# Kernel optimization log

Measured on AMD Instinct MI355X. Metric: run time of the kernel, lower is better.

## Reference

```python
import jax, jax.numpy as jnp
import numpy as np

N_NODES = 100000
IN_CH, HID_CH, OUT_CH = 128, 128, 64
N_EDGES = 1600000


def _gcn_conv(x, W, b, src, dst, num_nodes):
    """PyG GCNConv with gcn_norm(add_self_loops=True): adds one self-loop per
    node to the given edge set, symmetric deg^-1/2 normalization, then
    gather-scale-scatter of the linearly transformed features."""
    loop = jnp.arange(num_nodes)
    s = jnp.concatenate([src, loop])
    d = jnp.concatenate([dst, loop])
    # degree over targets (flow source_to_target), edge weights = 1
    deg = jax.ops.segment_sum(jnp.ones_like(s, x.dtype), d, num_segments=num_nodes)
    dinv = jnp.where(deg > 0, deg ** -0.5, 0.0)
    norm = dinv[s] * dinv[d]                      # [E']
    h = x @ W                                     # [N, out]
    msg = h[s] * norm[:, None]                    # [E', out] gather + scale
    out = jax.ops.segment_sum(msg, d, num_segments=num_nodes)  # scatter-add
    return out + b


def setup_inputs() -> dict:
    key = jax.random.key(0)
    k = jax.random.split(key, 6)
    x = jax.random.normal(k[0], (N_NODES, IN_CH), dtype=jnp.float32)
    edge_index = jax.random.randint(k[1], (2, N_EDGES), 0, N_NODES, dtype=jnp.int64)
    # Glorot-scale params
    W1 = jax.random.normal(k[2], (IN_CH, HID_CH), dtype=jnp.float32) * (2.0 / (IN_CH + HID_CH)) ** 0.5
    b1 = jnp.zeros((HID_CH,), dtype=jnp.float32)
    W2 = jax.random.normal(k[3], (HID_CH, OUT_CH), dtype=jnp.float32) * (2.0 / (HID_CH + OUT_CH)) ** 0.5
    b2 = jnp.zeros((OUT_CH,), dtype=jnp.float32)
    return {"x": x, "edge_index": edge_index, "W1": W1, "b1": b1, "W2": W2, "b2": b2}


def reference(x, edge_index, W1, b1, W2, b2):
    num_nodes = x.shape[0]
    loop = jnp.arange(num_nodes, dtype=edge_index.dtype)
    # wrapper-level add_self_loops (GCNConv adds another internally)
    src = jnp.concatenate([edge_index[0], loop])
    dst = jnp.concatenate([edge_index[1], loop])
    h = _gcn_conv(x, W1, b1, src, dst, num_nodes)
    h = jax.nn.relu(h)
    h = _gcn_conv(h, W2, b2, src, dst, num_nodes)
    return jax.nn.log_softmax(h, axis=1)
```

## Files before the change

kernel.cpp:

```cpp
#include <hip/hip_runtime.h>
#include <cstdint>
#include <cstddef>

#define IN_CH 128
#define HID_CH 128
#define OUT_CH 64
#define BSH 8
#define PB 4096
#define CAP 6144

typedef unsigned int uint32;
typedef unsigned char uchar;
typedef short bf16x8 __attribute__((ext_vector_type(8)));
typedef float f32x4 __attribute__((ext_vector_type(4)));
typedef float f32x2 __attribute__((ext_vector_type(2)));

static __device__ __forceinline__ unsigned short f2bf(float f) {
    uint32 u = __float_as_uint(f);
    u += 0x7fffu + ((u >> 16) & 1u);
    return (unsigned short)(u >> 16);
}

typedef const __attribute__((address_space(1))) char gch;
typedef __attribute__((address_space(3))) char lch;
static __device__ __forceinline__ void gload16(const void* g, void* l) {
    __builtin_amdgcn_global_load_lds((gch*)g, (lch*)l, 16, 0, 0);
}


__global__ __launch_bounds__(256) void part1_wtrans(
    const int* __restrict__ src, const int* __restrict__ dst,
    int* __restrict__ bcur, int2* __restrict__ pairBuf, int E, int NB, int gP,
    const float* __restrict__ W1, const float* __restrict__ W2,
    unsigned short* __restrict__ W1t, unsigned short* __restrict__ W2t) {
    if (blockIdx.x >= (uint32)gP) {
        int t = (blockIdx.x - gP) * 256 + threadIdx.x;
        if (t < 128 * 128) {
            int nc = t >> 7, k = t & 127;
            W1t[t] = f2bf(W1[k * 128 + nc]);
        }
        int u = t - 128 * 128;
        if (u >= 0 && u < 64 * 128) {
            int nc = u >> 7, k = u & 127;
            W2t[u] = f2bf(W2[k * 64 + nc]);
        }
        return;
    }
    __shared__ int2 pairs[PB];
    __shared__ int hist[512];
    __shared__ int base[512];
    int t = threadIdx.x;
    int e0 = blockIdx.x * PB;
    int cnt = min(PB, E - e0);
    for (int b = t; b < NB; b += 256) hist[b] = 0;
    __syncthreads();
    for (int i = t; i < cnt; i += 256) {
        int s = src[e0 + i], d = dst[e0 + i];
        pairs[i] = make_int2(s, d);
        atomicAdd(&hist[d >> BSH], 1);
    }
    __syncthreads();
    for (int b = t; b < NB; b += 256) {
        int h = hist[b];
        int gb = (h > 0) ? atomicAdd(&bcur[b], h) : 0;
        base[b] = b * CAP + gb;
        hist[b] = 0;
    }
    __syncthreads();
    for (int i = t; i < cnt; i += 256) {
        int2 p = pairs[i];
        int b = p.y >> BSH;
        int q = base[b] + atomicAdd(&hist[b], 1);
        pairBuf[q] = p;
    }
}

__global__ __launch_bounds__(256) void bucket_build(
    const int2* __restrict__ pairBuf, const int* __restrict__ bcur,
    int* __restrict__ rowptr, int* __restrict__ deg, float* __restrict__ dinv,
    int* __restrict__ csr, int N) {
    __shared__ int cnt[256];
    __shared__ int loc[256];
    int b = blockIdx.x, t = threadIdx.x;
    int start = b * CAP, end = start + bcur[b];
    cnt[t] = 0;
    __syncthreads();
    for (int i = start + t; i < end; i += 256)
        atomicAdd(&cnt[pairBuf[i].y & 255], 1);
    __syncthreads();
    int v = cnt[t];
    loc[t] = v;
    __syncthreads();
    for (int o = 1; o < 256; o <<= 1) {
        int add = (t >= o) ? loc[t - o] : 0;
        __syncthreads();
        loc[t] += add;
        __syncthreads();
    }
    int excl = loc[t] - v;
    int node = (b << BSH) + t;
    if (node < N) {
        rowptr[node] = start + excl;
        deg[node] = v;
        dinv[node] = rsqrtf((float)(v + 2));
    }
    __syncthreads();
    cnt[t] = excl;
    __syncthreads();
    for (int i = start + t; i < end; i += 256) {
        int2 p = pairBuf[i];
        int q = start + atomicAdd(&cnt[p.y & 255], 1);
        csr[q] = p.x;
    }
}


__global__ __launch_bounds__(256) void gemm1_mfma(
    const float* __restrict__ A, const unsigned short* __restrict__ Wt,
    const float* __restrict__ dinv, uchar* __restrict__ C, int n, int nTiles) {
    constexpr int NT = 8;
    constexpr int RP = 528;
    __shared__ unsigned short Ws[128 * 136];
    __shared__ char As[4 * 9216];

    const int t = threadIdx.x;

    for (int i = t; i < 128 * 16; i += 256) {
        int rr = i >> 4, sq = i & 15;
        *(uint4*)&Ws[rr * 136 + sq * 8] = *(const uint4*)(Wt + rr * 128 + sq * 8);
    }
    __syncthreads();

    const int w = t >> 6, l = t & 63;
    const int q = l >> 4, r16 = l & 15;
    char* slice = As + w * 9216;
    const char* myrow = slice + r16 * RP;

    for (int tile = blockIdx.x; tile < nTiles; tile += gridDim.x) {
        const int row0 = tile * 64 + w * 16;

#pragma unroll
        for (int rnd = 0; rnd < 9; rnd++) {
            int p = rnd * 1024 + l * 16;
            int row = p / RP;
            int col = (p - row * RP) & 511;
            int rg = min(row0 + min(row, 15), n - 1);
            gload16((const char*)A + (size_t)rg * 512 + col, slice + p);
        }
        asm volatile("s_waitcnt vmcnt(0)" ::: "memory");
        __builtin_amdgcn_sched_barrier(0);

        f32x4 acc[NT];
#pragma unroll
        for (int i = 0; i < NT; i++) acc[i] = (f32x4){0.f, 0.f, 0.f, 0.f};

#pragma unroll
        for (int s = 0; s < 4; s++) {
            const int k0 = s * 32 + q * 8;
            float4 v0 = *(const float4*)(myrow + k0 * 4);
            float4 v1 = *(const float4*)(myrow + k0 * 4 + 16);
            bf16x8 xf;
            xf[0] = (short)f2bf(v0.x); xf[1] = (short)f2bf(v0.y);
            xf[2] = (short)f2bf(v0.z); xf[3] = (short)f2bf(v0.w);
            xf[4] = (short)f2bf(v1.x); xf[5] = (short)f2bf(v1.y);
            xf[6] = (short)f2bf(v1.z); xf[7] = (short)f2bf(v1.w);
#pragma unroll
            for (int nt = 0; nt < NT; nt++) {
                bf16x8 wf = *(const bf16x8*)&Ws[(nt * 16 + r16) * 136 + k0];
                acc[nt] = __builtin_amdgcn_mfma_f32_16x16x32_bf16(wf, xf, acc[nt], 0, 0, 0);
            }
        }

        const int node = row0 + r16;
        const bool nv = node < n;
        const float dv = dinv[min(node, n - 1)];
        uchar* Crow = C + (size_t)node * 128;
#pragma unroll
        for (int nt = 0; nt < NT; nt++) {
            int pk = 0;
            pk = __builtin_amdgcn_cvt_pk_fp8_f32(acc[nt][0] * dv, acc[nt][1] * dv, pk, false);
            pk = __builtin_amdgcn_cvt_pk_fp8_f32(acc[nt][2] * dv, acc[nt][3] * dv, pk, true);
            if (nv) *(uint32*)(Crow + nt * 16 + q * 4) = (uint32)pk;
        }
    }
}


__global__ __launch_bounds__(256) void agg1_fused(
    const uchar* __restrict__ H, const int* __restrict__ csr,
    const int* __restrict__ rowptr, const int* __restrict__ deg,
    const float* __restrict__ dinv, const float* __restrict__ bias,
    const unsigned short* __restrict__ W2t, uchar* __restrict__ H2, int n) {
    __shared__ char stage[4][8192];
    __shared__ unsigned short tile[16 * 136];
    int t = threadIdx.x;
    int slot = t >> 4;
    int v = blockIdx.x * 16 + slot;
    int hl = t & 15;
    int gsel = t & 48;
    int w = t >> 6;
    int gg = (t >> 4) & 3;
    bool valid = v < n;
    int vc = valid ? v : 0;
    int base = rowptr[vc];
    int cnt = valid ? deg[vc] : 0;

    f32x2 A0 = (f32x2){0.f, 0.f}, A1 = A0, A2 = A0, A3 = A0;
    f32x2 B0 = A0, B1 = A0, B2 = A0, B3 = A0;

#define ACC128(h, s0, s1, s2, s3)                                   \
    {                                                               \
        s0 += __builtin_amdgcn_cvt_pk_f32_fp8((h).x, false);        \
        s1 += __builtin_amdgcn_cvt_pk_f32_fp8((h).x, true);         \
        s2 += __builtin_amdgcn_cvt_pk_f32_fp8((h).y, false);        \
        s3 += __builtin_amdgcn_cvt_pk_f32_fp8((h).y, true);         \
    }

    char* sl = stage[w];
    const char* rg = sl + gg * 256 + hl * 8;

    int ul = 0;
    if (hl < min(16, cnt)) ul = csr[base + hl];

    for (int j0 = 0; j0 < cnt; j0 += 16) {
        int nj = min(16, cnt - j0);
#pragma unroll
        for (int i = 0; i < 8; i++) {
            int j = i * 2 + (hl >> 3);
            int u = __shfl(ul, j | gsel);
            gload16(H + (((uint32)u << 7) + ((uint32)(hl & 7) << 4)),
                    sl + i * 1024);
        }
        int ul2 = 0;
        int j0n = j0 + 16;
        if (j0n < cnt && hl < min(16, cnt - j0n)) ul2 = csr[base + j0n + hl];
        asm volatile("s_waitcnt vmcnt(4)" ::: "memory");
        __builtin_amdgcn_sched_barrier(0);
#pragma unroll
        for (int j = 0; j < 8; j++) {
            if (j < nj) {
                uint2 h = *(const uint2*)(rg + (j >> 1) * 1024 + (j & 1) * 128);
                if (j & 1) { ACC128(h, B0, B1, B2, B3); }
                else       { ACC128(h, A0, A1, A2, A3); }
            }
        }
        asm volatile("s_waitcnt vmcnt(0)" ::: "memory");
        __builtin_amdgcn_sched_barrier(0);
#pragma unroll
        for (int j = 8; j < 16; j++) {
            if (j < nj) {
                uint2 h = *(const uint2*)(rg + (j >> 1) * 1024 + (j & 1) * 128);
                if (j & 1) { ACC128(h, B0, B1, B2, B3); }
                else       { ACC128(h, A0, A1, A2, A3); }
            }
        }
        ul = ul2;
    }
#undef ACC128

    const uint32 co = (uint32)(hl * 8);
    uint4 pk = make_uint4(0, 0, 0, 0);
    if (valid) {
        float dv = dinv[vc];
        uint2 hv = *(const uint2*)(H + (((uint32)vc << 7) + co));
        f32x2 s0 = __builtin_amdgcn_cvt_pk_f32_fp8(hv.x, false);
        f32x2 s1 = __builtin_amdgcn_cvt_pk_f32_fp8(hv.x, true);
        f32x2 s2 = __builtin_amdgcn_cvt_pk_f32_fp8(hv.y, false);
        f32x2 s3 = __builtin_amdgcn_cvt_pk_f32_fp8(hv.y, true);
        const f32x2* bp = (const f32x2*)(bias + hl * 8);
        f32x2 e0 = dv * ((A0 + B0) + 2.f * s0) + bp[0];
        f32x2 e1 = dv * ((A1 + B1) + 2.f * s1) + bp[1];
        f32x2 e2 = dv * ((A2 + B2) + 2.f * s2) + bp[2];
        f32x2 e3 = dv * ((A3 + B3) + 2.f * s3) + bp[3];
        float o0 = fmaxf(e0[0], 0.f), o1 = fmaxf(e0[1], 0.f);
        float o2 = fmaxf(e1[0], 0.f), o3 = fmaxf(e1[1], 0.f);
        float o4 = fmaxf(e2[0], 0.f), o5 = fmaxf(e2[1], 0.f);
        float o6 = fmaxf(e3[0], 0.f), o7 = fmaxf(e3[1], 0.f);
        pk.x = (uint32)f2bf(o0) | ((uint32)f2bf(o1) << 16);
        pk.y = (uint32)f2bf(o2) | ((uint32)f2bf(o3) << 16);
        pk.z = (uint32)f2bf(o4) | ((uint32)f2bf(o5) << 16);
        pk.w = (uint32)f2bf(o6) | ((uint32)f2bf(o7) << 16);
    }
    *(uint4*)&tile[slot * 136 + hl * 8] = pk;
    __syncthreads();

    const int l = t & 63;
    const int q = l >> 4, r16 = l & 15;
    f32x4 acc2 = (f32x4){0.f, 0.f, 0.f, 0.f};
#pragma unroll
    for (int s = 0; s < 4; s++) {
        const int k0 = s * 32 + q * 8;
        bf16x8 hf = *(const bf16x8*)&tile[r16 * 136 + k0];
        bf16x8 wf = *(const bf16x8*)(W2t + (size_t)(w * 16 + r16) * 128 + k0);
        acc2 = __builtin_amdgcn_mfma_f32_16x16x32_bf16(wf, hf, acc2, 0, 0, 0);
    }
    const int node = blockIdx.x * 16 + r16;
    if (node < n) {
        const float dv2 = dinv[node];
        int pk2 = 0;
        pk2 = __builtin_amdgcn_cvt_pk_fp8_f32(acc2[0] * dv2, acc2[1] * dv2, pk2, false);
        pk2 = __builtin_amdgcn_cvt_pk_fp8_f32(acc2[2] * dv2, acc2[3] * dv2, pk2, true);
        *(uint32*)(H2 + (size_t)node * 64 + w * 16 + q * 4) = (uint32)pk2;
    }
}

__global__ __launch_bounds__(256) void agg_lsm_64(
    const uchar* __restrict__ H, const int* __restrict__ csr,
    const int* __restrict__ rowptr, const int* __restrict__ deg,
    const float* __restrict__ dinv, const float* __restrict__ bias,
    float* __restrict__ out, int n) {
    __shared__ char stage[4][4096];
    int t = threadIdx.x;
    int v = blockIdx.x * 16 + (t >> 4);
    int hl = t & 15;
    int gsel = t & 48;
    int w = t >> 6;
    int gg = (t >> 4) & 3;
    bool valid = v < n;
    int vc = valid ? v : 0;
    int base = rowptr[vc];
    int cnt = valid ? deg[vc] : 0;
    const uint32 co = (uint32)(hl * 4);

    f32x2 A0 = (f32x2){0.f, 0.f}, A1 = A0, B0 = A0, B1 = A0;

#define ACC64(h, s0, s1)                                            \
    {                                                               \
        s0 += __builtin_amdgcn_cvt_pk_f32_fp8((h), false);          \
        s1 += __builtin_amdgcn_cvt_pk_f32_fp8((h), true);           \
    }

    char* sl = stage[w];
    const char* rg = sl + gg * 256 + hl * 4;

    int ul = 0;
    if (hl < min(16, cnt)) ul = csr[base + hl];

    for (int j0 = 0; j0 < cnt; j0 += 16) {
        int nj = min(16, cnt - j0);
#pragma unroll
        for (int i = 0; i < 4; i++) {
            int j = i * 4 + (hl >> 2);
            int u = __shfl(ul, j | gsel);
            gload16(H + (((uint32)u << 6) + ((uint32)(hl & 3) << 4)),
                    sl + i * 1024);
        }
        int ul2 = 0;
        int j0n = j0 + 16;
        if (j0n < cnt && hl < min(16, cnt - j0n)) ul2 = csr[base + j0n + hl];
        asm volatile("s_waitcnt vmcnt(2)" ::: "memory");
        __builtin_amdgcn_sched_barrier(0);
#pragma unroll
        for (int j = 0; j < 8; j++) {
            if (j < nj) {
                uint32 h = *(const uint32*)(rg + (j >> 2) * 1024 + (j & 3) * 64);
                if (j & 1) { ACC64(h, B0, B1); }
                else       { ACC64(h, A0, A1); }
            }
        }
        asm volatile("s_waitcnt vmcnt(0)" ::: "memory");
        __builtin_amdgcn_sched_barrier(0);
#pragma unroll
        for (int j = 8; j < 16; j++) {
            if (j < nj) {
                uint32 h = *(const uint32*)(rg + (j >> 2) * 1024 + (j & 3) * 64);
                if (j & 1) { ACC64(h, B0, B1); }
                else       { ACC64(h, A0, A1); }
            }
        }
        ul = ul2;
    }
#undef ACC64

    float dv = dinv[vc];
    uint32 hv = *(const uint32*)(H + (((uint32)vc << 6) + co));
    f32x2 s0 = __builtin_amdgcn_cvt_pk_f32_fp8(hv, false);
    f32x2 s1 = __builtin_amdgcn_cvt_pk_f32_fp8(hv, true);
    const f32x2* bp = (const f32x2*)(bias + hl * 4);
    f32x2 w0 = dv * ((A0 + B0) + 2.f * s0) + bp[0];
    f32x2 w1 = dv * ((A1 + B1) + 2.f * s1) + bp[1];
    float v0 = w0[0], v1 = w0[1], v2 = w1[0], v3 = w1[1];
    float m = fmaxf(fmaxf(v0, v1), fmaxf(v2, v3));
    for (int o = 8; o > 0; o >>= 1) m = fmaxf(m, __shfl_xor(m, o));
    float e = (__expf(v0 - m) + __expf(v1 - m)) + (__expf(v2 - m) + __expf(v3 - m));
    for (int o = 8; o > 0; o >>= 1) e += __shfl_xor(e, o);
    float ls = m + __logf(e);
    if (valid)
        *(float4*)(out + (size_t)vc * 64 + hl * 4) =
            make_float4(v0 - ls, v1 - ls, v2 - ls, v3 - ls);
}


extern "C" void kernel_launch(void* const* d_in, const int* in_sizes, int n_in,
                              void* d_out, int out_size, void* d_ws, size_t ws_size,
                              hipStream_t stream) {
    const float* x  = (const float*)d_in[0];
    const int*   ei = (const int*)d_in[1];
    const float* W1 = (const float*)d_in[2];
    const float* b1 = (const float*)d_in[3];
    const float* W2 = (const float*)d_in[4];
    const float* b2 = (const float*)d_in[5];
    float* out = (float*)d_out;

    const int N = in_sizes[0] / IN_CH;
    const int E = in_sizes[1] / 2;
    const int* src = ei;
    const int* dst = ei + E;
    const int NB = (N + 255) >> BSH;

    char* w = (char*)d_ws;
    size_t off = 0;
    auto alloc = [&](size_t bytes) -> char* {
        char* p = w + off;
        off = (off + bytes + 255) & ~(size_t)255;
        return p;
    };
    int*   deg    = (int*)alloc((size_t)N * 4);
    int*   rowptr = (int*)alloc((size_t)N * 4);
    int*   bcur   = (int*)alloc(512 * 4);
    float* dinv   = (float*)alloc((size_t)N * 4 + 1024);
    int*   csr    = (int*)alloc((size_t)NB * CAP * 4);
    unsigned short* W1t = (unsigned short*)alloc(128 * 128 * 2);
    unsigned short* W2t = (unsigned short*)alloc(64 * 128 * 2);
    uchar* H1  = (uchar*)alloc((size_t)N * HID_CH);
    char*  scratch = alloc((size_t)NB * CAP * 8);
    uchar* H2  = (uchar*)scratch;
    int2*  pairBuf = (int2*)scratch;

    hipMemsetAsync(bcur, 0, 512 * 4, stream);

    int gP = (E + PB - 1) / PB;

    part1_wtrans<<<gP + 96, 256, 0, stream>>>(src, dst, bcur, pairBuf, E, NB, gP,
                                              W1, W2, W1t, W2t);
    bucket_build<<<NB, 256, 0, stream>>>(pairBuf, bcur, rowptr, deg, dinv, csr, N);

    const int nTiles = (N + 63) / 64;
    const int gG = min(nTiles, 512);
    gemm1_mfma<<<gG, 256, 0, stream>>>(x, W1t, dinv, H1, N, nTiles);
    agg1_fused<<<(N + 15) / 16, 256, 0, stream>>>(H1, csr, rowptr, deg, dinv, b1, W2t, H2, N);
    agg_lsm_64<<<(N + 15) / 16, 256, 0, stream>>>(H2, csr, rowptr, deg, dinv, b2, out, N);
}
```

Before: 217.3 us.

## Compute degrees with global atomics and co-schedule edge partitioning with GEMM1

Degrees are now computed up front by a separate global-atomic histogram kernel, so the first GEMM no longer waits for bucket_build. Edge partitioning and GEMM1 run as disjoint block ranges of one launch so they can overlap. The dinv array is dropped and rsqrt(deg+2) is recomputed wherever it is needed. GEMM1 now reads W from global/L1 instead of staging it in LDS. The cost is 1.6M global atomics on deg plus an extra memset, and W reads lose LDS reuse.

```diff
diff --git a/kernel.cpp b/kernel.cpp
--- a/kernel.cpp
+++ b/kernel.cpp
@@ -28,13 +28,12 @@
 }
 
 
-__global__ __launch_bounds__(256) void part1_wtrans(
-    const int* __restrict__ src, const int* __restrict__ dst,
-    int* __restrict__ bcur, int2* __restrict__ pairBuf, int E, int NB, int gP,
+__global__ __launch_bounds__(256) void deg_wtrans(
+    const int* __restrict__ dst, int* __restrict__ deg, int E, int gD,
     const float* __restrict__ W1, const float* __restrict__ W2,
     unsigned short* __restrict__ W1t, unsigned short* __restrict__ W2t) {
-    if (blockIdx.x >= (uint32)gP) {
-        int t = (blockIdx.x - gP) * 256 + threadIdx.x;
+    if (blockIdx.x >= (uint32)gD) {
+        int t = (blockIdx.x - gD) * 256 + threadIdx.x;
         if (t < 128 * 128) {
             int nc = t >> 7, k = t & 127;
             W1t[t] = f2bf(W1[k * 128 + nc]);
@@ -46,97 +45,61 @@
         }
         return;
     }
-    __shared__ int2 pairs[PB];
-    __shared__ int hist[512];
-    __shared__ int base[512];
-    int t = threadIdx.x;
-    int e0 = blockIdx.x * PB;
-    int cnt = min(PB, E - e0);
-    for (int b = t; b < NB; b += 256) hist[b] = 0;
-    __syncthreads();
-    for (int i = t; i < cnt; i += 256) {
-        int s = src[e0 + i], d = dst[e0 + i];
-        pairs[i] = make_int2(s, d);
-        atomicAdd(&hist[d >> BSH], 1);
-    }
-    __syncthreads();
-    for (int b = t; b < NB; b += 256) {
-        int h = hist[b];
-        int gb = (h > 0) ? atomicAdd(&bcur[b], h) : 0;
-        base[b] = b * CAP + gb;
-        hist[b] = 0;
-    }
-    __syncthreads();
-    for (int i = t; i < cnt; i += 256) {
-        int2 p = pairs[i];
-        int b = p.y >> BSH;
-        int q = base[b] + atomicAdd(&hist[b], 1);
-        pairBuf[q] = p;
-    }
-}
-
-__global__ __launch_bounds__(256) void bucket_build(
-    const int2* __restrict__ pairBuf, const int* __restrict__ bcur,
-    int* __restrict__ rowptr, int* __restrict__ deg, float* __restrict__ dinv,
-    int* __restrict__ csr, int N) {
-    __shared__ int cnt[256];
-    __shared__ int loc[256];
-    int b = blockIdx.x, t = threadIdx.x;
-    int start = b * CAP, end = start + bcur[b];
-    cnt[t] = 0;
-    __syncthreads();
-    for (int i = start + t; i < end; i += 256)
-        atomicAdd(&cnt[pairBuf[i].y & 255], 1);
-    __syncthreads();
-    int v = cnt[t];
-    loc[t] = v;
-    __syncthreads();
-    for (int o = 1; o < 256; o <<= 1) {
-        int add = (t >= o) ? loc[t - o] : 0;
+    int i0 = blockIdx.x * 256 + threadIdx.x;
+    int stride = gD * 256;
+    for (int i = i0; i < E; i += stride)
+        atomicAdd(&deg[dst[i]], 1);
+}
+
+
+__global__ __launch_bounds__(256) void fused_p1g1(
+    const int* __restrict__ src, const int* __restrict__ dst,
+    int* __restrict__ bcur, int2* __restrict__ pairBuf, int E, int NB, int gP,
+    const float* __restrict__ A, const unsigned short* __restrict__ Wt,
+    const int* __restrict__ deg, uchar* __restrict__ C, int n, int nTiles, int gG) {
+    __shared__ char smem[36864];
+    const int t = threadIdx.x;
+
+    if (blockIdx.x < (uint32)gP) {
+        int2* pairs = (int2*)smem;
+        int* hist = (int*)(smem + 32768);
+        int* base = (int*)(smem + 34816);
+        int e0 = blockIdx.x * PB;
+        int cnt = min(PB, E - e0);
+        for (int b = t; b < NB; b += 256) hist[b] = 0;
         __syncthreads();
-        loc[t] += add;
+        for (int i = t; i < cnt; i += 256) {
+            int s = src[e0 + i], d = dst[e0 + i];
+            pairs[i] = make_int2(s, d);
+            atomicAdd(&hist[d >> BSH], 1);
+        }
         __syncthreads();
-    }
-    int excl = loc[t] - v;
-    int node = (b << BSH) + t;
-    if (node < N) {
-        rowptr[node] = start + excl;
-        deg[node] = v;
-        dinv[node] = rsqrtf((float)(v + 2));
-    }
-    __syncthreads();
-    cnt[t] = excl;
-    __syncthreads();
-    for (int i = start + t; i < end; i += 256) {
-        int2 p = pairBuf[i];
-        int q = start + atomicAdd(&cnt[p.y & 255], 1);
-        csr[q] = p.x;
-    }
-}
-
-
-__global__ __launch_bounds__(256) void gemm1_mfma(
-    const float* __restrict__ A, const unsigned short* __restrict__ Wt,
-    const float* __restrict__ dinv, uchar* __restrict__ C, int n, int nTiles) {
+        for (int b = t; b < NB; b += 256) {
+            int h = hist[b];
+            int gb = (h > 0) ? atomicAdd(&bcur[b], h) : 0;
+            base[b] = b * CAP + gb;
+            hist[b] = 0;
+        }
+        __syncthreads();
+        for (int i = t; i < cnt; i += 256) {
+            int2 p = pairs[i];
+            int b = p.y >> BSH;
+            int q = base[b] + atomicAdd(&hist[b], 1);
+            pairBuf[q] = p;
+        }
+        return;
+    }
+
     constexpr int NT = 8;
     constexpr int RP = 528;
-    __shared__ unsigned short Ws[128 * 136];
-    __shared__ char As[4 * 9216];
-
-    const int t = threadIdx.x;
-
-    for (int i = t; i < 128 * 16; i += 256) {
-        int rr = i >> 4, sq = i & 15;
-        *(uint4*)&Ws[rr * 136 + sq * 8] = *(const uint4*)(Wt + rr * 128 + sq * 8);
-    }
-    __syncthreads();
+    char* As = smem;
 
     const int w = t >> 6, l = t & 63;
     const int q = l >> 4, r16 = l & 15;
     char* slice = As + w * 9216;
     const char* myrow = slice + r16 * RP;
 
-    for (int tile = blockIdx.x; tile < nTiles; tile += gridDim.x) {
+    for (int tile = blockIdx.x - gP; tile < nTiles; tile += gG) {
         const int row0 = tile * 64 + w * 16;
 
 #pragma unroll
@@ -166,14 +129,14 @@
             xf[6] = (short)f2bf(v1.z); xf[7] = (short)f2bf(v1.w);
 #pragma unroll
             for (int nt = 0; nt < NT; nt++) {
-                bf16x8 wf = *(const bf16x8*)&Ws[(nt * 16 + r16) * 136 + k0];
+                bf16x8 wf = *(const bf16x8*)(Wt + (size_t)(nt * 16 + r16) * 128 + k0);
                 acc[nt] = __builtin_amdgcn_mfma_f32_16x16x32_bf16(wf, xf, acc[nt], 0, 0, 0);
             }
         }
 
         const int node = row0 + r16;
         const bool nv = node < n;
-        const float dv = dinv[min(node, n - 1)];
+        const float dv = rsqrtf((float)(deg[min(node, n - 1)] + 2));
         uchar* Crow = C + (size_t)node * 128;
 #pragma unroll
         for (int nt = 0; nt < NT; nt++) {
@@ -186,10 +149,40 @@
 }
 
 
+__global__ __launch_bounds__(256) void bucket_build(
+    const int2* __restrict__ pairBuf, const int* __restrict__ bcur,
+    const int* __restrict__ deg, int* __restrict__ rowptr,
+    int* __restrict__ csr, int N) {
+    __shared__ int cnt[256];
+    __shared__ int loc[256];
+    int b = blockIdx.x, t = threadIdx.x;
+    int start = b * CAP, end = start + bcur[b];
+    int node = (b << BSH) + t;
+    int v = (node < N) ? deg[node] : 0;
+    loc[t] = v;
+    __syncthreads();
+    for (int o = 1; o < 256; o <<= 1) {
+        int add = (t >= o) ? loc[t - o] : 0;
+        __syncthreads();
+        loc[t] += add;
+        __syncthreads();
+    }
+    int excl = loc[t] - v;
+    if (node < N) rowptr[node] = start + excl;
+    cnt[t] = excl;
+    __syncthreads();
+    for (int i = start + t; i < end; i += 256) {
+        int2 p = pairBuf[i];
+        int q = start + atomicAdd(&cnt[p.y & 255], 1);
+        csr[q] = p.x;
+    }
+}
+
+
 __global__ __launch_bounds__(256) void agg1_fused(
     const uchar* __restrict__ H, const int* __restrict__ csr,
     const int* __restrict__ rowptr, const int* __restrict__ deg,
-    const float* __restrict__ dinv, const float* __restrict__ bias,
+    const float* __restrict__ bias,
     const unsigned short* __restrict__ W2t, uchar* __restrict__ H2, int n) {
     __shared__ char stage[4][8192];
     __shared__ unsigned short tile[16 * 136];
@@ -261,7 +254,7 @@
     const uint32 co = (uint32)(hl * 8);
     uint4 pk = make_uint4(0, 0, 0, 0);
     if (valid) {
-        float dv = dinv[vc];
+        float dv = rsqrtf((float)(cnt + 2));
         uint2 hv = *(const uint2*)(H + (((uint32)vc << 7) + co));
         f32x2 s0 = __builtin_amdgcn_cvt_pk_f32_fp8(hv.x, false);
         f32x2 s1 = __builtin_amdgcn_cvt_pk_f32_fp8(hv.x, true);
@@ -296,7 +289,7 @@
     }
     const int node = blockIdx.x * 16 + r16;
     if (node < n) {
-        const float dv2 = dinv[node];
+        const float dv2 = rsqrtf((float)(deg[node] + 2));
         int pk2 = 0;
         pk2 = __builtin_amdgcn_cvt_pk_fp8_f32(acc2[0] * dv2, acc2[1] * dv2, pk2, false);
         pk2 = __builtin_amdgcn_cvt_pk_fp8_f32(acc2[2] * dv2, acc2[3] * dv2, pk2, true);
@@ -307,8 +300,7 @@
 __global__ __launch_bounds__(256) void agg_lsm_64(
     const uchar* __restrict__ H, const int* __restrict__ csr,
     const int* __restrict__ rowptr, const int* __restrict__ deg,
-    const float* __restrict__ dinv, const float* __restrict__ bias,
-    float* __restrict__ out, int n) {
+    const float* __restrict__ bias, float* __restrict__ out, int n) {
     __shared__ char stage[4][4096];
     int t = threadIdx.x;
     int v = blockIdx.x * 16 + (t >> 4);
@@ -372,7 +364,7 @@
     }
 #undef ACC64
 
-    float dv = dinv[vc];
+    float dv = rsqrtf((float)(cnt + 2));
     uint32 hv = *(const uint32*)(H + (((uint32)vc << 6) + co));
     f32x2 s0 = __builtin_amdgcn_cvt_pk_f32_fp8(hv, false);
     f32x2 s1 = __builtin_amdgcn_cvt_pk_f32_fp8(hv, true);
@@ -418,7 +410,6 @@
     int*   deg    = (int*)alloc((size_t)N * 4);
     int*   rowptr = (int*)alloc((size_t)N * 4);
     int*   bcur   = (int*)alloc(512 * 4);
-    float* dinv   = (float*)alloc((size_t)N * 4 + 1024);
     int*   csr    = (int*)alloc((size_t)NB * CAP * 4);
     unsigned short* W1t = (unsigned short*)alloc(128 * 128 * 2);
     unsigned short* W2t = (unsigned short*)alloc(64 * 128 * 2);
@@ -427,17 +418,18 @@
     uchar* H2  = (uchar*)scratch;
     int2*  pairBuf = (int2*)scratch;
 
+    hipMemsetAsync(deg, 0, (size_t)N * 4, stream);
     hipMemsetAsync(bcur, 0, 512 * 4, stream);
 
-    int gP = (E + PB - 1) / PB;
-
-    part1_wtrans<<<gP + 96, 256, 0, stream>>>(src, dst, bcur, pairBuf, E, NB, gP,
-                                              W1, W2, W1t, W2t);
-    bucket_build<<<NB, 256, 0, stream>>>(pairBuf, bcur, rowptr, deg, dinv, csr, N);
-
+    const int gD = 1024;
+    const int gP = (E + PB - 1) / PB;
     const int nTiles = (N + 63) / 64;
-    const int gG = min(nTiles, 512);
-    gemm1_mfma<<<gG, 256, 0, stream>>>(x, W1t, dinv, H1, N, nTiles);
-    agg1_fused<<<(N + 15) / 16, 256, 0, stream>>>(H1, csr, rowptr, deg, dinv, b1, W2t, H2, N);
-    agg_lsm_64<<<(N + 15) / 16, 256, 0, stream>>>(H2, csr, rowptr, deg, dinv, b2, out, N);
-}
+    const int gG = 512;
+
+    deg_wtrans<<<gD + 96, 256, 0, stream>>>(dst, deg, E, gD, W1, W2, W1t, W2t);
+    fused_p1g1<<<gP + gG, 256, 0, stream>>>(src, dst, bcur, pairBuf, E, NB, gP,
+                                            x, W1t, deg, H1, N, nTiles, gG);
+    bucket_build<<<NB, 256, 0, stream>>>(pairBuf, bcur, deg, rowptr, csr, N);
+    agg1_fused<<<(N + 15) / 16, 256, 0, stream>>>(H1, csr, rowptr, deg, b1, W2t, H2, N);
+    agg_lsm_64<<<(N + 15) / 16, 256, 0, stream>>>(H2, csr, rowptr, deg, b2, out, N);
+}
```

Measured after the change: 288.5 us. 32.8% more time.
